# Optimization experiments

Hardware: AMD Instinct MI355X
Metric: run time of the kernel (lower is better)

The kernel has to match this reference:

```python
import jax, jax.numpy as jnp
import numpy as np

HD = 256          # hidden_dim[0]
KF = 2            # k factor
KD = HD * KF      # 512, bilinear feature dim
L = 2000          # hard-coded sequence length
B = 4
NEG = np.float32(np.finfo(np.float32).min)  # finite min, NOT -inf (matches torch code)
EPS = 1e-5


def _fc(x, V, g, b):
    # weight_norm(Linear, dim=None): W = g * V / ||V||_F, then ReLU
    W = (g / jnp.linalg.norm(V)) * V  # [KD, HD]
    return jax.nn.relu(jnp.einsum('blh,kh->blk', x, W) + b)


def setup_inputs() -> dict:
    key = jax.random.key(0)
    ks = jax.random.split(key, 12)
    X = jax.random.normal(ks[0], (B, L, HD), dtype=jnp.float32)
    Y = jax.random.normal(ks[1], (B, L, HD), dtype=jnp.float32)
    mask1 = jax.random.bernoulli(ks[2], 0.8, (B, L)).astype(jnp.float32)
    mask2 = jax.random.bernoulli(ks[3], 0.8, (B, L)).astype(jnp.float32)
    # Q_net / K_net params (single weight-normed linear each)
    Qv = jax.random.normal(ks[4], (KD, HD), dtype=jnp.float32) * 0.05
    Qg = jnp.asarray(1.0, dtype=jnp.float32)
    Qb = jax.random.normal(ks[5], (KD,), dtype=jnp.float32) * 0.05
    Kv = jax.random.normal(ks[6], (KD, HD), dtype=jnp.float32) * 0.05
    Kg = jnp.asarray(1.0, dtype=jnp.float32)
    Kb = jax.random.normal(ks[7], (KD,), dtype=jnp.float32) * 0.05
    h_mat = jax.random.normal(ks[8], (KD,), dtype=jnp.float32)   # (1,1,KD) squeezed
    h_bias = jax.random.normal(ks[9], (), dtype=jnp.float32)     # (1,1,1) squeezed
    gamma = jnp.ones((KD,), dtype=jnp.float32)                   # BatchNorm1d affine
    beta = jnp.zeros((KD,), dtype=jnp.float32)
    return {"X": X, "Y": Y, "mask1": mask1, "mask2": mask2,
            "Qv": Qv, "Qg": Qg, "Qb": Qb, "Kv": Kv, "Kg": Kg, "Kb": Kb,
            "h_mat": h_mat, "h_bias": h_bias, "gamma": gamma, "beta": beta}


def _masked_softmax(A, m_row):
    # m_row: [B,1,L], broadcasts over axis 1; softmax over dim 1 as in torch
    logits = jnp.where(m_row > 0, A, NEG)
    att = jax.nn.softmax(logits, axis=1)
    return m_row * att


def reference(X, Y, mask1, mask2, Qv, Qg, Qb, Kv, Kg, Kb, h_mat, h_bias, gamma, beta):
    A1_X = _fc(X, Qv, Qg, Qb)  # [B,L,KD]
    A1_Y = _fc(Y, Kv, Kg, Kb)
    A2_Y = _fc(Y, Qv, Qg, Qb)
    A2_X = _fc(X, Kv, Kg, Kb)
    # bilinear co-attention maps [B,L,L]
    A1 = jnp.einsum('bvk,bqk->bvq', A1_X * h_mat, A1_Y) + h_bias
    A2 = jnp.einsum('bqk,bvk->bqv', A2_Y * h_mat, A2_X) + h_bias
    m1r = mask1[:, None, :]  # mask1_attend[b,v,q] = mask1[b,q]
    m2r = mask2[:, None, :]
    alpha = _masked_softmax(A1, m2r)
    logits_X = jnp.einsum('bvq,bqk->bvk', alpha, A1_Y) * mask1[:, :, None]
    beta_att = _masked_softmax(A2, m1r)
    logits_Y = jnp.einsum('bqv,bvk->bqk', beta_att, A2_X) * mask2[:, :, None]
    # AvgPool2d((2000,1)) == mean over sequence dim
    pooled = logits_X.mean(axis=1) + logits_Y.mean(axis=1)  # [B,KD]
    # BatchNorm1d training-mode forward (biased batch stats)
    mu = pooled.mean(axis=0)
    var = pooled.var(axis=0)
    return gamma * (pooled - mu) * jax.lax.rsqrt(var + EPS) + beta
```

## Files before the change

### kernel.cpp

```cpp
#include <hip/hip_runtime.h>

#define NB 4
#define LSEQ 2000
#define HD 256
#define KD 512
#define LPAD 2048
#define SMALL_N 18562

using short8 = __attribute__((ext_vector_type(8))) short;
using f32x4  = __attribute__((ext_vector_type(4))) float;
typedef unsigned short u16;

__device__ __forceinline__ float b2f(u16 u) { return __uint_as_float(((unsigned)u) << 16); }
__device__ __forceinline__ u16 f2b(float f) {
    unsigned u = __float_as_uint(f);
    u += 0x7FFFu + ((u >> 16) & 1u);
    return (u16)(u >> 16);
}
__device__ __forceinline__ bool detect32(const void* gamma) {
    return ((const float*)gamma)[0] == 1.0f;
}
__device__ __forceinline__ void gl_lds16(const u16* g, short* l) {
    __builtin_amdgcn_global_load_lds(
        (const __attribute__((address_space(1))) unsigned int*)g,
        (__attribute__((address_space(3))) unsigned int*)l, 16, 0, 0);
}

__global__ void convert_kernel(const void* X, const void* Y, const void* Qv, const void* Kv,
                               const void* m1, const void* m2, const void* Qb, const void* Kb,
                               const void* hm, const void* Qg, const void* Kg,
                               const void* gamma, const void* beta,
                               u16* __restrict__ Xb, u16* __restrict__ Yb,
                               u16* __restrict__ Qvb, u16* __restrict__ Kvb,
                               float* __restrict__ smallf, float* __restrict__ ssq)
{
    const bool is32 = detect32(gamma);
    const int seg = blockIdx.y;
    if (seg < 4) {
        const void* src = seg == 0 ? X : seg == 1 ? Y : seg == 2 ? Qv : Kv;
        u16* dst = seg == 0 ? Xb : seg == 1 ? Yb : seg == 2 ? Qvb : Kvb;
        const int n = (seg < 2) ? NB * LSEQ * HD : KD * HD;
        const int i0 = (blockIdx.x * 256 + threadIdx.x) * 8;
        if (i0 >= n) return;
        uint4 pack;
        u16* v = (u16*)&pack;
        if (is32) {
            float4 fa = ((const float4*)src)[(i0 >> 2)];
            float4 fb = ((const float4*)src)[(i0 >> 2) + 1];
            v[0] = f2b(fa.x); v[1] = f2b(fa.y); v[2] = f2b(fa.z); v[3] = f2b(fa.w);
            v[4] = f2b(fb.x); v[5] = f2b(fb.y); v[6] = f2b(fb.z); v[7] = f2b(fb.w);
        } else {
            pack = ((const uint4*)src)[i0 >> 3];
        }
        ((uint4*)dst)[i0 >> 3] = pack;
        if (seg >= 2) {
            float s = 0.f;
            #pragma unroll
            for (int j = 0; j < 8; ++j) { float f = b2f(v[j]); s = fmaf(f, f, s); }
            #pragma unroll
            for (int off = 32; off > 0; off >>= 1) s += __shfl_xor(s, off);
            if ((threadIdx.x & 63) == 0) atomicAdd(&ssq[seg - 2], s);
        }
    } else {
        const int i0 = (blockIdx.x * 256 + threadIdx.x) * 4;
        for (int i = i0; i < i0 + 4; ++i) {
            if (i >= SMALL_N) break;
            const void* src; int off;
            if      (i <  8000) { src = m1;    off = i; }
            else if (i < 16000) { src = m2;    off = i - 8000; }
            else if (i < 16512) { src = Qb;    off = i - 16000; }
            else if (i < 17024) { src = Kb;    off = i - 16512; }
            else if (i < 17536) { src = hm;    off = i - 17024; }
            else if (i < 18048) { src = gamma; off = i - 17536; }
            else if (i < 18560) { src = beta;  off = i - 18048; }
            else if (i == 18560) {
                float f = ((const float*)Qg)[0];
                smallf[i] = (f == 1.0f) ? 1.0f : b2f(((const u16*)Qg)[0]);
                continue;
            } else {
                float f = ((const float*)Kg)[0];
                smallf[i] = (f == 1.0f) ? 1.0f : b2f(((const u16*)Kg)[0]);
                continue;
            }
            smallf[i] = is32 ? ((const float*)src)[off] : b2f(((const u16*)src)[off]);
        }
    }
}

__global__ __launch_bounds__(256, 2)
void fc_kernel(const u16* __restrict__ X, const u16* __restrict__ Y,
               const u16* __restrict__ Qv, const u16* __restrict__ Kv,
               const float* __restrict__ Qbf, const float* __restrict__ Kbf,
               const float* __restrict__ hf, const float* __restrict__ gv,
               const float* __restrict__ ssq, u16* __restrict__ fc)
{
    const int mt = blockIdx.x, nt = blockIdx.y, t = blockIdx.z;
    const int b = t >> 2, which = t & 3;
    const u16* In = ((which == 0) | (which == 3)) ? (X + (size_t)b * LSEQ * HD)
                                                  : (Y + (size_t)b * LSEQ * HD);
    const bool isQ = (which == 0) | (which == 2);
    const u16* W      = isQ ? Qv : Kv;
    const float* bias = isQ ? Qbf : Kbf;
    const int j = isQ ? 0 : 1;
    const float s = gv[j] / sqrtf(ssq[j]);
    u16* out = fc + (size_t)t * LSEQ * KD;

    __shared__ __align__(16) short As[2][128 * 32];
    __shared__ __align__(16) short Bs[2][128 * 32];

    const int tid = threadIdx.x;
    const int lane = tid & 63, wave = tid >> 6;
    const int wm = wave >> 1, wn = wave & 1;
    const int quad = lane >> 4, l15 = lane & 15;
    const int sr = tid >> 2, sc = tid & 3;
    const int scz = sc ^ ((sr >> 1) & 3);
    const int m0 = mt * 128, n0 = nt * 128;

    int gm0 = min(m0 + sr, LSEQ - 1), gm1 = min(m0 + sr + 64, LSEQ - 1);
    const u16* pA0 = In + (size_t)gm0 * HD + scz * 8;
    const u16* pA1 = In + (size_t)gm1 * HD + scz * 8;
    const u16* pB0 = W + (size_t)(n0 + sr) * HD + scz * 8;
    const u16* pB1 = W + (size_t)(n0 + sr + 64) * HD + scz * 8;
    const int dof = sr * 32 + sc * 8;

    int aoff[4], boff[4];
    #pragma unroll
    for (int i = 0; i < 4; ++i) {
        int ra = wm * 64 + i * 16 + l15;
        aoff[i] = ra * 32 + (quad ^ ((ra >> 1) & 3)) * 8;
        int rb = wn * 64 + i * 16 + l15;
        boff[i] = rb * 32 + (quad ^ ((rb >> 1) & 3)) * 8;
    }

    gl_lds16(pA0, &As[0][dof]);
    gl_lds16(pA1, &As[0][64 * 32 + dof]);
    gl_lds16(pB0, &Bs[0][dof]);
    gl_lds16(pB1, &Bs[0][64 * 32 + dof]);
    __syncthreads();

    f32x4 acc[4][4] = {};

    for (int kt = 0; kt < 8; ++kt) {
        const int cur = kt & 1, nxt = cur ^ 1;
        if (kt < 7) {
            const int ko = (kt + 1) * 32;
            gl_lds16(pA0 + ko, &As[nxt][dof]);
            gl_lds16(pA1 + ko, &As[nxt][64 * 32 + dof]);
            gl_lds16(pB0 + ko, &Bs[nxt][dof]);
            gl_lds16(pB1 + ko, &Bs[nxt][64 * 32 + dof]);
        }
        short8 af[4], bf[4];
        #pragma unroll
        for (int i = 0; i < 4; ++i) af[i] = *(const short8*)&As[cur][aoff[i]];
        #pragma unroll
        for (int i = 0; i < 4; ++i) bf[i] = *(const short8*)&Bs[cur][boff[i]];
        #pragma unroll
        for (int mi = 0; mi < 4; ++mi)
            #pragma unroll
            for (int ni = 0; ni < 4; ++ni)
                acc[mi][ni] = __builtin_amdgcn_mfma_f32_16x16x32_bf16(af[mi], bf[ni], acc[mi][ni], 0, 0, 0);
        __syncthreads();
    }

    #pragma unroll
    for (int ni = 0; ni < 4; ++ni) {
        int n = n0 + wn * 64 + ni * 16 + l15;
        float bv = bias[n];
        float hv = isQ ? hf[n] : 1.0f;
        #pragma unroll
        for (int mi = 0; mi < 4; ++mi) {
            int mb = m0 + wm * 64 + mi * 16 + quad * 4;
            #pragma unroll
            for (int r = 0; r < 4; ++r) {
                int m = mb + r;
                if (m < LSEQ) {
                    float v = fmaf(s, acc[mi][ni][r], bv);
                    v = v > 0.f ? v : 0.f;
                    out[(size_t)m * KD + n] = f2b(v * hv);
                }
            }
        }
    }
}

__global__ __launch_bounds__(256, 2)
void colsm_kernel(const u16* __restrict__ fc, const float* __restrict__ m1f,
                  const float* __restrict__ m2f,
                  float* __restrict__ part_d, float* __restrict__ part_n)
{
    const int vs = blockIdx.x, qt = blockIdx.y, z = blockIdx.z;
    const int a = z >> 2, b = z & 3;
    const u16* R  = fc + (size_t)(b * 4 + (a == 0 ? 1 : 3)) * LSEQ * KD;
    const u16* Sm = fc + (size_t)(b * 4 + (a == 0 ? 0 : 2)) * LSEQ * KD;
    const float* wmask = (a == 0 ? m1f : m2f) + (size_t)b * LSEQ;

    __shared__ __align__(16) short Rs[2][128 * 32];
    __shared__ __align__(16) short Ss[2][128 * 32];
    __shared__ float ldsD[128][2];
    __shared__ float ldsN[128][2];

    const int tid = threadIdx.x;
    const int lane = tid & 63, wave = tid >> 6;
    const int wrow = wave >> 1, wcol = wave & 1;
    const int quad = lane >> 4, l15 = lane & 15;
    const int sr = tid >> 2, sc = tid & 3;
    const int scz = sc ^ ((sr >> 1) & 3);
    const int r0 = qt * 128, c0 = vs * 128;

    int gr0 = min(r0 + sr, LSEQ - 1), gr1 = min(r0 + sr + 64, LSEQ - 1);
    int gc0 = min(c0 + sr, LSEQ - 1), gc1 = min(c0 + sr + 64, LSEQ - 1);
    const u16* pR0 = R  + (size_t)gr0 * KD + scz * 8;
    const u16* pR1 = R  + (size_t)gr1 * KD + scz * 8;
    const u16* pS0 = Sm + (size_t)gc0 * KD + scz * 8;
    const u16* pS1 = Sm + (size_t)gc1 * KD + scz * 8;
    const int dof = sr * 32 + sc * 8;

    int aoff[4], boff[4];
    #pragma unroll
    for (int i = 0; i < 4; ++i) {
        int ra = wrow * 64 + i * 16 + l15;
        aoff[i] = ra * 32 + (quad ^ ((ra >> 1) & 3)) * 8;
        int rb = wcol * 64 + i * 16 + l15;
        boff[i] = rb * 32 + (quad ^ ((rb >> 1) & 3)) * 8;
    }

    gl_lds16(pR0, &Rs[0][dof]);
    gl_lds16(pR1, &Rs[0][64 * 32 + dof]);
    gl_lds16(pS0, &Ss[0][dof]);
    gl_lds16(pS1, &Ss[0][64 * 32 + dof]);
    __syncthreads();

    f32x4 acc[4][4] = {};

    for (int kt = 0; kt < 16; ++kt) {
        const int cur = kt & 1, nxt = cur ^ 1;
        if (kt < 15) {
            const int ko = (kt + 1) * 32;
            gl_lds16(pR0 + ko, &Rs[nxt][dof]);
            gl_lds16(pR1 + ko, &Rs[nxt][64 * 32 + dof]);
            gl_lds16(pS0 + ko, &Ss[nxt][dof]);
            gl_lds16(pS1 + ko, &Ss[nxt][64 * 32 + dof]);
        }
        short8 af[4], bf[4];
        #pragma unroll
        for (int i = 0; i < 4; ++i) af[i] = *(const short8*)&Rs[cur][aoff[i]];
        #pragma unroll
        for (int i = 0; i < 4; ++i) bf[i] = *(const short8*)&Ss[cur][boff[i]];
        #pragma unroll
        for (int mi = 0; mi < 4; ++mi)
            #pragma unroll
            for (int ni = 0; ni < 4; ++ni)
                acc[mi][ni] = __builtin_amdgcn_mfma_f32_16x16x32_bf16(af[mi], bf[ni], acc[mi][ni], 0, 0, 0);
        __syncthreads();
    }

    float wv[4], vv[4];
    #pragma unroll
    for (int ni = 0; ni < 4; ++ni) {
        int cg = c0 + wcol * 64 + ni * 16 + l15;
        bool valid = cg < LSEQ;
        vv[ni] = valid ? 1.f : 0.f;
        wv[ni] = valid ? wmask[cg] : 0.f;
    }
    #pragma unroll
    for (int mi = 0; mi < 4; ++mi)
        #pragma unroll
        for (int r = 0; r < 4; ++r) {
            float d = 0.f, n = 0.f;
            #pragma unroll
            for (int ni = 0; ni < 4; ++ni) {
                float e = __expf(acc[mi][ni][r]);
                d = fmaf(vv[ni], e, d);
                n = fmaf(wv[ni], e, n);
            }
            #pragma unroll
            for (int off = 1; off < 16; off <<= 1) {
                d += __shfl_xor(d, off);
                n += __shfl_xor(n, off);
            }
            if (l15 == 0) {
                int row = wrow * 64 + mi * 16 + quad * 4 + r;
                ldsD[row][wcol] = d;
                ldsN[row][wcol] = n;
            }
        }
    __syncthreads();
    if (tid < 128) {
        int q = r0 + tid;
        if (q < LSEQ) {
            size_t p = ((size_t)(z * 16 + vs)) * LPAD + q;
            part_d[p] = ldsD[tid][0] + ldsD[tid][1];
            part_n[p] = ldsN[tid][0] + ldsN[tid][1];
        }
    }
}

__global__ void combine_kernel(const float* __restrict__ part_d, const float* __restrict__ part_n,
                               const float* __restrict__ m1f, const float* __restrict__ m2f,
                               float* __restrict__ c, float* __restrict__ pooled)
{
    int idx = blockIdx.x * 256 + threadIdx.x;
    if (idx < NB * KD) pooled[idx] = 0.f;
    int z = idx >> 11, q = idx & (LPAD - 1);
    int a = z >> 2, b = z & 3;
    float d = 0.f, n = 0.f;
    #pragma unroll
    for (int vs = 0; vs < 16; ++vs) {
        size_t p = ((size_t)(z * 16 + vs)) * LPAD + q;
        d += part_d[p]; n += part_n[p];
    }
    float val = 0.f;
    if (q < LSEQ) {
        float om = (a == 0 ? m2f : m1f)[b * LSEQ + q];
        val = om * n / d;
    }
    c[(size_t)z * LPAD + q] = val;
}

__global__ void pooled_kernel(const u16* __restrict__ fc, const float* __restrict__ c,
                              float* __restrict__ pooled)
{
    const int b = blockIdx.x, rs = blockIdx.y;
    const int k = threadIdx.x;
    const u16* YK = fc + (size_t)(b * 4 + 1) * LSEQ * KD;
    const u16* XK = fc + (size_t)(b * 4 + 3) * LSEQ * KD;
    const float* c1 = c + (size_t)(0 + b) * LPAD;
    const float* c2 = c + (size_t)(4 + b) * LPAD;
    float s = 0.f;
    const int rbeg = rs * 50, rend = rbeg + 50;
    for (int r = rbeg; r < rend; ++r) {
        s = fmaf(c1[r], b2f(YK[(size_t)r * KD + k]), s);
        s = fmaf(c2[r], b2f(XK[(size_t)r * KD + k]), s);
    }
    atomicAdd(&pooled[b * KD + k], s * (1.0f / LSEQ));
}

__global__ void ln_kernel(const float* __restrict__ pooled, const float* __restrict__ gammaf,
                          const float* __restrict__ betaf, const void* __restrict__ gamma_orig,
                          void* __restrict__ out)
{
    int k = blockIdx.x * 256 + threadIdx.x;
    float p[NB];
    #pragma unroll
    for (int b = 0; b < NB; ++b) p[b] = pooled[b * KD + k];
    float mu = 0.25f * (p[0] + p[1] + p[2] + p[3]);
    float var = 0.f;
    #pragma unroll
    for (int b = 0; b < NB; ++b) { float d = p[b] - mu; var = fmaf(d, d, var); }
    var *= 0.25f;
    float inv = rsqrtf(var + 1e-5f);
    float g = gammaf[k], be = betaf[k];
    const bool is32 = detect32(gamma_orig);
    #pragma unroll
    for (int b = 0; b < NB; ++b) {
        float v = fmaf(g * (p[b] - mu), inv, be);
        if (is32) ((float*)out)[b * KD + k] = v;
        else      ((u16*)out)[b * KD + k] = f2b(v);
    }
}

extern "C" void kernel_launch(void* const* d_in, const int* in_sizes, int n_in,
                              void* d_out, int out_size, void* d_ws, size_t ws_size,
                              hipStream_t stream)
{
    const void* X  = d_in[0];
    const void* Y  = d_in[1];
    const void* m1 = d_in[2];
    const void* m2 = d_in[3];
    const void* Qv = d_in[4];
    const void* Qg = d_in[5];
    const void* Qb = d_in[6];
    const void* Kv = d_in[7];
    const void* Kg = d_in[8];
    const void* Kb = d_in[9];
    const void* h  = d_in[10];
    const void* gamma = d_in[12];
    const void* beta  = d_in[13];

    char* ws = (char*)d_ws;
    size_t off = 0;
    u16* Xb  = (u16*)(ws + off); off += (size_t)NB * LSEQ * HD * 2;
    u16* Yb  = (u16*)(ws + off); off += (size_t)NB * LSEQ * HD * 2;
    u16* Qvb = (u16*)(ws + off); off += (size_t)KD * HD * 2;
    u16* Kvb = (u16*)(ws + off); off += (size_t)KD * HD * 2;
    float* smallf = (float*)(ws + off); off += ((size_t)(SMALL_N + 2) * 4 + 15) / 16 * 16;
    u16* fc  = (u16*)(ws + off); off += (size_t)16 * LSEQ * KD * 2;
    float* part_d = (float*)(ws + off); off += (size_t)8 * 16 * LPAD * 4;
    float* part_n = (float*)(ws + off); off += (size_t)8 * 16 * LPAD * 4;
    float* c      = (float*)(ws + off); off += (size_t)8 * LPAD * 4;
    float* pooled = (float*)(ws + off); off += (size_t)NB * KD * 4;

    const float* m1f = smallf;
    const float* m2f = smallf + 8000;
    const float* Qbf = smallf + 16000;
    const float* Kbf = smallf + 16512;
    const float* hf  = smallf + 17024;
    const float* gmf = smallf + 17536;
    const float* bef = smallf + 18048;
    const float* gv  = smallf + 18560;
    float* ssq = smallf + SMALL_N;

    hipMemsetAsync(ssq, 0, 2 * sizeof(float), stream);
    convert_kernel<<<dim3(1000, 5), 256, 0, stream>>>(X, Y, Qv, Kv, m1, m2, Qb, Kb, h, Qg, Kg,
                                                      gamma, beta, Xb, Yb, Qvb, Kvb, smallf, ssq);
    fc_kernel     <<<dim3(16, 4, 16), 256, 0, stream>>>(Xb, Yb, Qvb, Kvb, Qbf, Kbf, hf, gv, ssq, fc);
    colsm_kernel  <<<dim3(16, 16, 8), 256, 0, stream>>>(fc, m1f, m2f, part_d, part_n);
    combine_kernel<<<64, 256, 0, stream>>>(part_d, part_n, m1f, m2f, c, pooled);
    pooled_kernel <<<dim3(4, 40), 512, 0, stream>>>(fc, c, pooled);
    ln_kernel     <<<2, 256, 0, stream>>>(pooled, gmf, bef, gamma, d_out);
}
```

Measured before the change: 197.3 us.

## Load GEMM fragments directly from global into registers, vectorize pooled reduction

The fc and colsm GEMM kernels drop their LDS double buffers and barriers. Each wave now loads its MFMA fragments straight from global memory into registers, prefetched two k-steps ahead. This removes LDS traffic and __syncthreads, but each block reads its A and B tiles redundantly across waves and relies on L1/L2 for reuse, with higher register pressure. The pooled kernel is also rewritten to use 16-byte vector loads of 8 bf16 values per thread, with fewer blocks and threads.

```diff
diff --git a/kernel.cpp b/kernel.cpp
--- a/kernel.cpp
+++ b/kernel.cpp
@@ -19,11 +19,6 @@
 }
 __device__ __forceinline__ bool detect32(const void* gamma) {
     return ((const float*)gamma)[0] == 1.0f;
-}
-__device__ __forceinline__ void gl_lds16(const u16* g, short* l) {
-    __builtin_amdgcn_global_load_lds(
-        (const __attribute__((address_space(1))) unsigned int*)g,
-        (__attribute__((address_space(3))) unsigned int*)l, 16, 0, 0);
 }
 
 __global__ void convert_kernel(const void* X, const void* Y, const void* Qv, const void* Kv,
@@ -87,7 +82,7 @@
     }
 }
 
-__global__ __launch_bounds__(256, 2)
+__global__ __launch_bounds__(256)
 void fc_kernel(const u16* __restrict__ X, const u16* __restrict__ Y,
                const u16* __restrict__ Qv, const u16* __restrict__ Kv,
                const float* __restrict__ Qbf, const float* __restrict__ Kbf,
@@ -105,61 +100,50 @@
     const float s = gv[j] / sqrtf(ssq[j]);
     u16* out = fc + (size_t)t * LSEQ * KD;
 
-    __shared__ __align__(16) short As[2][128 * 32];
-    __shared__ __align__(16) short Bs[2][128 * 32];
-
     const int tid = threadIdx.x;
     const int lane = tid & 63, wave = tid >> 6;
     const int wm = wave >> 1, wn = wave & 1;
     const int quad = lane >> 4, l15 = lane & 15;
-    const int sr = tid >> 2, sc = tid & 3;
-    const int scz = sc ^ ((sr >> 1) & 3);
     const int m0 = mt * 128, n0 = nt * 128;
 
-    int gm0 = min(m0 + sr, LSEQ - 1), gm1 = min(m0 + sr + 64, LSEQ - 1);
-    const u16* pA0 = In + (size_t)gm0 * HD + scz * 8;
-    const u16* pA1 = In + (size_t)gm1 * HD + scz * 8;
-    const u16* pB0 = W + (size_t)(n0 + sr) * HD + scz * 8;
-    const u16* pB1 = W + (size_t)(n0 + sr + 64) * HD + scz * 8;
-    const int dof = sr * 32 + sc * 8;
-
-    int aoff[4], boff[4];
+    const u16* pa[4]; const u16* pb[4];
     #pragma unroll
     for (int i = 0; i < 4; ++i) {
-        int ra = wm * 64 + i * 16 + l15;
-        aoff[i] = ra * 32 + (quad ^ ((ra >> 1) & 3)) * 8;
-        int rb = wn * 64 + i * 16 + l15;
-        boff[i] = rb * 32 + (quad ^ ((rb >> 1) & 3)) * 8;
-    }
-
-    gl_lds16(pA0, &As[0][dof]);
-    gl_lds16(pA1, &As[0][64 * 32 + dof]);
-    gl_lds16(pB0, &Bs[0][dof]);
-    gl_lds16(pB1, &Bs[0][64 * 32 + dof]);
-    __syncthreads();
+        int ra = min(m0 + wm * 64 + i * 16 + l15, LSEQ - 1);
+        pa[i] = In + (size_t)ra * HD + quad * 8;
+        int cb = n0 + wn * 64 + i * 16 + l15;
+        pb[i] = W + (size_t)cb * HD + quad * 8;
+    }
+
+    short8 fA[2][4], fB[2][4];
+    #pragma unroll
+    for (int i = 0; i < 4; ++i) {
+        fA[0][i] = *(const short8*)(pa[i]);
+        fB[0][i] = *(const short8*)(pb[i]);
+        fA[1][i] = *(const short8*)(pa[i] + 32);
+        fB[1][i] = *(const short8*)(pb[i] + 32);
+    }
 
     f32x4 acc[4][4] = {};
-
+    #pragma unroll 2
     for (int kt = 0; kt < 8; ++kt) {
-        const int cur = kt & 1, nxt = cur ^ 1;
-        if (kt < 7) {
-            const int ko = (kt + 1) * 32;
-            gl_lds16(pA0 + ko, &As[nxt][dof]);
-            gl_lds16(pA1 + ko, &As[nxt][64 * 32 + dof]);
-            gl_lds16(pB0 + ko, &Bs[nxt][dof]);
-            gl_lds16(pB1 + ko, &Bs[nxt][64 * 32 + dof]);
-        }
-        short8 af[4], bf[4];
-        #pragma unroll
-        for (int i = 0; i < 4; ++i) af[i] = *(const short8*)&As[cur][aoff[i]];
-        #pragma unroll
-        for (int i = 0; i < 4; ++i) bf[i] = *(const short8*)&Bs[cur][boff[i]];
+        const int cur = kt & 1;
+        short8 a_[4], b_[4];
+        #pragma unroll
+        for (int i = 0; i < 4; ++i) { a_[i] = fA[cur][i]; b_[i] = fB[cur][i]; }
+        if (kt + 2 < 8) {
+            const int ko = (kt + 2) * 32;
+            #pragma unroll
+            for (int i = 0; i < 4; ++i) {
+                fA[cur][i] = *(const short8*)(pa[i] + ko);
+                fB[cur][i] = *(const short8*)(pb[i] + ko);
+            }
+        }
         #pragma unroll
         for (int mi = 0; mi < 4; ++mi)
             #pragma unroll
             for (int ni = 0; ni < 4; ++ni)
-                acc[mi][ni] = __builtin_amdgcn_mfma_f32_16x16x32_bf16(af[mi], bf[ni], acc[mi][ni], 0, 0, 0);
-        __syncthreads();
+                acc[mi][ni] = __builtin_amdgcn_mfma_f32_16x16x32_bf16(a_[mi], b_[ni], acc[mi][ni], 0, 0, 0);
     }
 
     #pragma unroll
@@ -183,7 +167,7 @@
     }
 }
 
-__global__ __launch_bounds__(256, 2)
+__global__ __launch_bounds__(256)
 void colsm_kernel(const u16* __restrict__ fc, const float* __restrict__ m1f,
                   const float* __restrict__ m2f,
                   float* __restrict__ part_d, float* __restrict__ part_n)
@@ -194,8 +178,6 @@
     const u16* Sm = fc + (size_t)(b * 4 + (a == 0 ? 0 : 2)) * LSEQ * KD;
     const float* wmask = (a == 0 ? m1f : m2f) + (size_t)b * LSEQ;
 
-    __shared__ __align__(16) short Rs[2][128 * 32];
-    __shared__ __align__(16) short Ss[2][128 * 32];
     __shared__ float ldsD[128][2];
     __shared__ float ldsN[128][2];
 
@@ -203,55 +185,46 @@
     const int lane = tid & 63, wave = tid >> 6;
     const int wrow = wave >> 1, wcol = wave & 1;
     const int quad = lane >> 4, l15 = lane & 15;
-    const int sr = tid >> 2, sc = tid & 3;
-    const int scz = sc ^ ((sr >> 1) & 3);
     const int r0 = qt * 128, c0 = vs * 128;
 
-    int gr0 = min(r0 + sr, LSEQ - 1), gr1 = min(r0 + sr + 64, LSEQ - 1);
-    int gc0 = min(c0 + sr, LSEQ - 1), gc1 = min(c0 + sr + 64, LSEQ - 1);
-    const u16* pR0 = R  + (size_t)gr0 * KD + scz * 8;
-    const u16* pR1 = R  + (size_t)gr1 * KD + scz * 8;
-    const u16* pS0 = Sm + (size_t)gc0 * KD + scz * 8;
-    const u16* pS1 = Sm + (size_t)gc1 * KD + scz * 8;
-    const int dof = sr * 32 + sc * 8;
-
-    int aoff[4], boff[4];
+    const u16* pa[4]; const u16* pb[4];
     #pragma unroll
     for (int i = 0; i < 4; ++i) {
-        int ra = wrow * 64 + i * 16 + l15;
-        aoff[i] = ra * 32 + (quad ^ ((ra >> 1) & 3)) * 8;
-        int rb = wcol * 64 + i * 16 + l15;
-        boff[i] = rb * 32 + (quad ^ ((rb >> 1) & 3)) * 8;
-    }
-
-    gl_lds16(pR0, &Rs[0][dof]);
-    gl_lds16(pR1, &Rs[0][64 * 32 + dof]);
-    gl_lds16(pS0, &Ss[0][dof]);
-    gl_lds16(pS1, &Ss[0][64 * 32 + dof]);
-    __syncthreads();
+        int ra = min(r0 + wrow * 64 + i * 16 + l15, LSEQ - 1);
+        pa[i] = R + (size_t)ra * KD + quad * 8;
+        int cb = min(c0 + wcol * 64 + i * 16 + l15, LSEQ - 1);
+        pb[i] = Sm + (size_t)cb * KD + quad * 8;
+    }
+
+    short8 fA[2][4], fB[2][4];
+    #pragma unroll
+    for (int i = 0; i < 4; ++i) {
+        fA[0][i] = *(const short8*)(pa[i]);
+        fB[0][i] = *(const short8*)(pb[i]);
+        fA[1][i] = *(const short8*)(pa[i] + 32);
+        fB[1][i] = *(const short8*)(pb[i] + 32);
+    }
 
     f32x4 acc[4][4] = {};
-
+    #pragma unroll 2
     for (int kt = 0; kt < 16; ++kt) {
-        const int cur = kt & 1, nxt = cur ^ 1;
-        if (kt < 15) {
-            const int ko = (kt + 1) * 32;
-            gl_lds16(pR0 + ko, &Rs[nxt][dof]);
-            gl_lds16(pR1 + ko, &Rs[nxt][64 * 32 + dof]);
-            gl_lds16(pS0 + ko, &Ss[nxt][dof]);
-            gl_lds16(pS1 + ko, &Ss[nxt][64 * 32 + dof]);
-        }
-        short8 af[4], bf[4];
-        #pragma unroll
-        for (int i = 0; i < 4; ++i) af[i] = *(const short8*)&Rs[cur][aoff[i]];
-        #pragma unroll
-        for (int i = 0; i < 4; ++i) bf[i] = *(const short8*)&Ss[cur][boff[i]];
+        const int cur = kt & 1;
+        short8 a_[4], b_[4];
+        #pragma unroll
+        for (int i = 0; i < 4; ++i) { a_[i] = fA[cur][i]; b_[i] = fB[cur][i]; }
+        if (kt + 2 < 16) {
+            const int ko = (kt + 2) * 32;
+            #pragma unroll
+            for (int i = 0; i < 4; ++i) {
+                fA[cur][i] = *(const short8*)(pa[i] + ko);
+                fB[cur][i] = *(const short8*)(pb[i] + ko);
+            }
+        }
         #pragma unroll
         for (int mi = 0; mi < 4; ++mi)
             #pragma unroll
             for (int ni = 0; ni < 4; ++ni)
-                acc[mi][ni] = __builtin_amdgcn_mfma_f32_16x16x32_bf16(af[mi], bf[ni], acc[mi][ni], 0, 0, 0);
-        __syncthreads();
+                acc[mi][ni] = __builtin_amdgcn_mfma_f32_16x16x32_bf16(a_[mi], b_[ni], acc[mi][ni], 0, 0, 0);
     }
 
     float wv[4], vv[4];
@@ -321,18 +294,27 @@
                               float* __restrict__ pooled)
 {
     const int b = blockIdx.x, rs = blockIdx.y;
-    const int k = threadIdx.x;
+    const int k8 = (threadIdx.x & 63) * 8;
+    const int rg = threadIdx.x >> 6;
     const u16* YK = fc + (size_t)(b * 4 + 1) * LSEQ * KD;
     const u16* XK = fc + (size_t)(b * 4 + 3) * LSEQ * KD;
     const float* c1 = c + (size_t)(0 + b) * LPAD;
     const float* c2 = c + (size_t)(4 + b) * LPAD;
-    float s = 0.f;
-    const int rbeg = rs * 50, rend = rbeg + 50;
+    float s[8] = {};
+    const int rbeg = rs * 200 + rg * 50, rend = rbeg + 50;
     for (int r = rbeg; r < rend; ++r) {
-        s = fmaf(c1[r], b2f(YK[(size_t)r * KD + k]), s);
-        s = fmaf(c2[r], b2f(XK[(size_t)r * KD + k]), s);
-    }
-    atomicAdd(&pooled[b * KD + k], s * (1.0f / LSEQ));
+        float w1 = c1[r], w2 = c2[r];
+        uint4 uy = *(const uint4*)(YK + (size_t)r * KD + k8);
+        uint4 ux = *(const uint4*)(XK + (size_t)r * KD + k8);
+        const u16* py = (const u16*)&uy;
+        const u16* px = (const u16*)&ux;
+        #pragma unroll
+        for (int j = 0; j < 8; ++j)
+            s[j] = fmaf(w1, b2f(py[j]), fmaf(w2, b2f(px[j]), s[j]));
+    }
+    #pragma unroll
+    for (int j = 0; j < 8; ++j)
+        atomicAdd(&pooled[b * KD + k8 + j], s[j] * (1.0f / LSEQ));
 }
 
 __global__ void ln_kernel(const float* __restrict__ pooled, const float* __restrict__ gammaf,
@@ -406,6 +388,6 @@
     fc_kernel     <<<dim3(16, 4, 16), 256, 0, stream>>>(Xb, Yb, Qvb, Kvb, Qbf, Kbf, hf, gv, ssq, fc);
     colsm_kernel  <<<dim3(16, 16, 8), 256, 0, stream>>>(fc, m1f, m2f, part_d, part_n);
     combine_kernel<<<64, 256, 0, stream>>>(part_d, part_n, m1f, m2f, c, pooled);
-    pooled_kernel <<<dim3(4, 40), 512, 0, stream>>>(fc, c, pooled);
+    pooled_kernel <<<dim3(4, 10), 256, 0, stream>>>(fc, c, pooled);
     ln_kernel     <<<2, 256, 0, stream>>>(pooled, gmf, bef, gamma, d_out);
 }
```

Result: slower. 330.0 us (+67.3%).

## Fuse combine into pooled kernel, drop memset, swizzle block order

Applied to the files above, without the earlier changes.

Merges the partial-sum combine step into the pooled reduction kernel, which now loads the combined weights into shared memory and reads rows with vectorized 16-byte loads, one kernel per 8 columns. The Frobenius-norm atomics are replaced by per-block partial sums that each fc block reduces itself. The memset is removed and the pooled buffer is zeroed inside the convert kernel. fc and colsm grids are flattened with an index order that interleaves batches and operand sets, likely for better cache locality across concurrently running blocks. This trades two launches and a memset for redundant 64-element reductions in every fc block.

```diff
diff --git a/kernel.cpp b/kernel.cpp
--- a/kernel.cpp
+++ b/kernel.cpp
@@ -32,7 +32,8 @@
                                const void* gamma, const void* beta,
                                u16* __restrict__ Xb, u16* __restrict__ Yb,
                                u16* __restrict__ Qvb, u16* __restrict__ Kvb,
-                               float* __restrict__ smallf, float* __restrict__ ssq)
+                               float* __restrict__ smallf, float* __restrict__ ssqp,
+                               float* __restrict__ pooled)
 {
     const bool is32 = detect32(gamma);
     const int seg = blockIdx.y;
@@ -59,10 +60,17 @@
             for (int j = 0; j < 8; ++j) { float f = b2f(v[j]); s = fmaf(f, f, s); }
             #pragma unroll
             for (int off = 32; off > 0; off >>= 1) s += __shfl_xor(s, off);
-            if ((threadIdx.x & 63) == 0) atomicAdd(&ssq[seg - 2], s);
+            __shared__ float red[4];
+            if ((threadIdx.x & 63) == 0) red[threadIdx.x >> 6] = s;
+            __syncthreads();
+            if (threadIdx.x == 0)
+                ssqp[(seg - 2) * 64 + blockIdx.x] = red[0] + red[1] + red[2] + red[3];
         }
     } else {
         const int i0 = (blockIdx.x * 256 + threadIdx.x) * 4;
+        #pragma unroll
+        for (int j = 0; j < 4; ++j)
+            if (i0 + j < NB * KD) pooled[i0 + j] = 0.f;
         for (int i = i0; i < i0 + 4; ++i) {
             if (i >= SMALL_N) break;
             const void* src; int off;
@@ -92,9 +100,13 @@
                const u16* __restrict__ Qv, const u16* __restrict__ Kv,
                const float* __restrict__ Qbf, const float* __restrict__ Kbf,
                const float* __restrict__ hf, const float* __restrict__ gv,
-               const float* __restrict__ ssq, u16* __restrict__ fc)
-{
-    const int mt = blockIdx.x, nt = blockIdx.y, t = blockIdx.z;
+               const float* __restrict__ ssqp, u16* __restrict__ fc)
+{
+    const int id = blockIdx.x;
+    const int z7 = id & 7, idx = id >> 3;
+    const int t = z7 + 8 * (idx & 1);
+    const int tile = idx >> 1;
+    const int mt = tile & 15, nt = tile >> 4;
     const int b = t >> 2, which = t & 3;
     const u16* In = ((which == 0) | (which == 3)) ? (X + (size_t)b * LSEQ * HD)
                                                   : (Y + (size_t)b * LSEQ * HD);
@@ -102,7 +114,9 @@
     const u16* W      = isQ ? Qv : Kv;
     const float* bias = isQ ? Qbf : Kbf;
     const int j = isQ ? 0 : 1;
-    const float s = gv[j] / sqrtf(ssq[j]);
+    float ssq = 0.f;
+    for (int i = 0; i < 64; ++i) ssq += ssqp[j * 64 + i];
+    const float s = gv[j] / sqrtf(ssq);
     u16* out = fc + (size_t)t * LSEQ * KD;
 
     __shared__ __align__(16) short As[2][128 * 32];
@@ -188,7 +202,9 @@
                   const float* __restrict__ m2f,
                   float* __restrict__ part_d, float* __restrict__ part_n)
 {
-    const int vs = blockIdx.x, qt = blockIdx.y, z = blockIdx.z;
+    const int id = blockIdx.x;
+    const int z = id & 7, rem = id >> 3;
+    const int vs = rem & 15, qt = rem >> 4;
     const int a = z >> 2, b = z & 3;
     const u16* R  = fc + (size_t)(b * 4 + (a == 0 ? 1 : 3)) * LSEQ * KD;
     const u16* Sm = fc + (size_t)(b * 4 + (a == 0 ? 0 : 2)) * LSEQ * KD;
@@ -295,44 +311,50 @@
     }
 }
 
-__global__ void combine_kernel(const float* __restrict__ part_d, const float* __restrict__ part_n,
+__global__ void pooledc_kernel(const u16* __restrict__ fc,
+                               const float* __restrict__ part_d, const float* __restrict__ part_n,
                                const float* __restrict__ m1f, const float* __restrict__ m2f,
-                               float* __restrict__ c, float* __restrict__ pooled)
-{
-    int idx = blockIdx.x * 256 + threadIdx.x;
-    if (idx < NB * KD) pooled[idx] = 0.f;
-    int z = idx >> 11, q = idx & (LPAD - 1);
-    int a = z >> 2, b = z & 3;
-    float d = 0.f, n = 0.f;
-    #pragma unroll
-    for (int vs = 0; vs < 16; ++vs) {
-        size_t p = ((size_t)(z * 16 + vs)) * LPAD + q;
-        d += part_d[p]; n += part_n[p];
-    }
-    float val = 0.f;
-    if (q < LSEQ) {
-        float om = (a == 0 ? m2f : m1f)[b * LSEQ + q];
-        val = om * n / d;
-    }
-    c[(size_t)z * LPAD + q] = val;
-}
-
-__global__ void pooled_kernel(const u16* __restrict__ fc, const float* __restrict__ c,
-                              float* __restrict__ pooled)
+                               float* __restrict__ pooled)
 {
     const int b = blockIdx.x, rs = blockIdx.y;
-    const int k = threadIdx.x;
+    const int tid = threadIdx.x;
+    __shared__ float c1s[200], c2s[200];
+
+    if (tid < 200) {
+        int r = rs * 200 + tid;
+        float d1 = 0.f, n1 = 0.f, d2 = 0.f, n2 = 0.f;
+        #pragma unroll
+        for (int vs = 0; vs < 16; ++vs) {
+            size_t p1 = ((size_t)(b * 16 + vs)) * LPAD + r;
+            size_t p2 = ((size_t)((4 + b) * 16 + vs)) * LPAD + r;
+            d1 += part_d[p1]; n1 += part_n[p1];
+            d2 += part_d[p2]; n2 += part_n[p2];
+        }
+        c1s[tid] = m2f[b * LSEQ + r] * n1 / d1;
+        c2s[tid] = m1f[b * LSEQ + r] * n2 / d2;
+    }
+    __syncthreads();
+
+    const int k8 = (tid & 63) * 8;
+    const int rg = tid >> 6;
     const u16* YK = fc + (size_t)(b * 4 + 1) * LSEQ * KD;
     const u16* XK = fc + (size_t)(b * 4 + 3) * LSEQ * KD;
-    const float* c1 = c + (size_t)(0 + b) * LPAD;
-    const float* c2 = c + (size_t)(4 + b) * LPAD;
-    float s = 0.f;
-    const int rbeg = rs * 50, rend = rbeg + 50;
-    for (int r = rbeg; r < rend; ++r) {
-        s = fmaf(c1[r], b2f(YK[(size_t)r * KD + k]), s);
-        s = fmaf(c2[r], b2f(XK[(size_t)r * KD + k]), s);
-    }
-    atomicAdd(&pooled[b * KD + k], s * (1.0f / LSEQ));
+    float s[8] = {};
+    const int lbeg = rg * 50, lend = lbeg + 50;
+    for (int lr = lbeg; lr < lend; ++lr) {
+        int r = rs * 200 + lr;
+        float w1 = c1s[lr], w2 = c2s[lr];
+        uint4 uy = *(const uint4*)(YK + (size_t)r * KD + k8);
+        uint4 ux = *(const uint4*)(XK + (size_t)r * KD + k8);
+        const u16* py = (const u16*)&uy;
+        const u16* px = (const u16*)&ux;
+        #pragma unroll
+        for (int j = 0; j < 8; ++j)
+            s[j] = fmaf(w1, b2f(py[j]), fmaf(w2, b2f(px[j]), s[j]));
+    }
+    #pragma unroll
+    for (int j = 0; j < 8; ++j)
+        atomicAdd(&pooled[b * KD + k8 + j], s[j] * (1.0f / LSEQ));
 }
 
 __global__ void ln_kernel(const float* __restrict__ pooled, const float* __restrict__ gammaf,
@@ -383,11 +405,11 @@
     u16* Yb  = (u16*)(ws + off); off += (size_t)NB * LSEQ * HD * 2;
     u16* Qvb = (u16*)(ws + off); off += (size_t)KD * HD * 2;
     u16* Kvb = (u16*)(ws + off); off += (size_t)KD * HD * 2;
-    float* smallf = (float*)(ws + off); off += ((size_t)(SMALL_N + 2) * 4 + 15) / 16 * 16;
+    float* smallf = (float*)(ws + off); off += ((size_t)SMALL_N * 4 + 15) / 16 * 16;
+    float* ssqp   = (float*)(ws + off); off += 128 * 4;
     u16* fc  = (u16*)(ws + off); off += (size_t)16 * LSEQ * KD * 2;
     float* part_d = (float*)(ws + off); off += (size_t)8 * 16 * LPAD * 4;
     float* part_n = (float*)(ws + off); off += (size_t)8 * 16 * LPAD * 4;
-    float* c      = (float*)(ws + off); off += (size_t)8 * LPAD * 4;
     float* pooled = (float*)(ws + off); off += (size_t)NB * KD * 4;
 
     const float* m1f = smallf;
@@ -398,14 +420,12 @@
     const float* gmf = smallf + 17536;
     const float* bef = smallf + 18048;
     const float* gv  = smallf + 18560;
-    float* ssq = smallf + SMALL_N;
-
-    hipMemsetAsync(ssq, 0, 2 * sizeof(float), stream);
+
     convert_kernel<<<dim3(1000, 5), 256, 0, stream>>>(X, Y, Qv, Kv, m1, m2, Qb, Kb, h, Qg, Kg,
-                                                      gamma, beta, Xb, Yb, Qvb, Kvb, smallf, ssq);
-    fc_kernel     <<<dim3(16, 4, 16), 256, 0, stream>>>(Xb, Yb, Qvb, Kvb, Qbf, Kbf, hf, gv, ssq, fc);
-    colsm_kernel  <<<dim3(16, 16, 8), 256, 0, stream>>>(fc, m1f, m2f, part_d, part_n);
-    combine_kernel<<<64, 256, 0, stream>>>(part_d, part_n, m1f, m2f, c, pooled);
-    pooled_kernel <<<dim3(4, 40), 512, 0, stream>>>(fc, c, pooled);
+                                                      gamma, beta, Xb, Yb, Qvb, Kvb,
+                                                      smallf, ssqp, pooled);
+    fc_kernel     <<<1024, 256, 0, stream>>>(Xb, Yb, Qvb, Kvb, Qbf, Kbf, hf, gv, ssqp, fc);
+    colsm_kernel  <<<2048, 256, 0, stream>>>(fc, m1f, m2f, part_d, part_n);
+    pooledc_kernel<<<dim3(4, 10), 256, 0, stream>>>(fc, part_d, part_n, m1f, m2f, pooled);
     ln_kernel     <<<2, 256, 0, stream>>>(pooled, gmf, bef, gamma, d_out);
 }
```

Result: slower. 202.1 us (+2.4%).
